# Performance work log

Hardware: AMD Instinct MI355X
Metric: run time of the kernel (lower is better)

The kernel has to match this reference:

```python
import jax, jax.numpy as jnp
import numpy as np


def _lstm_scan(x_tbd, h0, c0, Wi, Wh, b):
    # x_tbd: [T, B, D]; standard LSTMCell, gate order i, f, g, o.
    def step(carry, xt):
        h, c = carry
        gates = xt @ Wi.T + h @ Wh.T + b  # [B, 4H]
        i, f, g, o = jnp.split(gates, 4, axis=-1)
        c = jax.nn.sigmoid(f) * c + jax.nn.sigmoid(i) * jnp.tanh(g)
        h = jax.nn.sigmoid(o) * jnp.tanh(c)
        return (h, c), h
    _, ys = jax.lax.scan(step, (h0, c0), x_tbd)
    return ys  # [T, B, H]


def setup_inputs() -> dict:
    key = jax.random.key(0)
    ks = jax.random.split(key, 8)
    B, T, D, H = 64, 512, 512, 512
    inputs_emb = jax.random.normal(ks[0], (B, T, D), dtype=jnp.float32)
    # variable sequence lengths in [T//2, T], mask = 1 for valid positions
    lengths = jax.random.randint(ks[1], (B,), T // 2, T + 1)
    mask = (jnp.arange(T)[None, :] < lengths[:, None]).astype(jnp.float32)
    s = 1.0 / np.sqrt(H)
    return {
        "inputs_emb": inputs_emb,
        "mask": mask,
        "h0": jnp.zeros((B, H), jnp.float32),
        "c0": jnp.zeros((B, H), jnp.float32),
        "Wi_f": jax.random.uniform(ks[2], (4 * H, D), jnp.float32, -s, s),
        "Wh_f": jax.random.uniform(ks[3], (4 * H, H), jnp.float32, -s, s),
        "b_f": jnp.zeros((4 * H,), jnp.float32),
        "Wi_b": jax.random.uniform(ks[4], (4 * H, D), jnp.float32, -s, s),
        "Wh_b": jax.random.uniform(ks[5], (4 * H, H), jnp.float32, -s, s),
        "b_b": jnp.zeros((4 * H,), jnp.float32),
    }


def reference(inputs_emb, mask, h0, c0, Wi_f, Wh_f, b_f, Wi_b, Wh_b, b_b):
    B, T, D = inputs_emb.shape
    # ---- forward direction ----
    ys_f = _lstm_scan(inputs_emb.transpose(1, 0, 2), h0, c0, Wi_f, Wh_f, b_f)  # [T,B,H]
    out_f = ys_f.transpose(1, 0, 2)  # [B,T,H]
    # ---- backward direction with gather-based reordering ----
    lengths = mask.astype(jnp.int32).sum(axis=1)  # [B]
    t_idx = jnp.arange(T)[None, :]
    # index_b: rotate so padding comes first: [len..T-1] ++ [0..len-1]
    idx_b = (t_idx + lengths[:, None]) % T  # [B,T]
    # index_f: rotate back: [T-len..T-1] ++ [0..T-len-1]
    idx_f = (t_idx + (T - lengths)[:, None]) % T  # [B,T]
    x_b = jnp.take_along_axis(inputs_emb, idx_b[:, :, None], axis=1)  # [B,T,D]
    # run cell over reversed time, then reverse collected outputs back
    x_b_rev = x_b.transpose(1, 0, 2)[::-1]  # [T,B,D], t = T-1 .. 0
    ys_b_rev = _lstm_scan(x_b_rev, h0, c0, Wi_b, Wh_b, b_b)  # [T,B,H]
    out_b = ys_b_rev[::-1].transpose(1, 0, 2)  # [B,T,H], time order
    out_b = jnp.take_along_axis(out_b, idx_f[:, :, None], axis=1)
    return jnp.concatenate([out_f, out_b], axis=-1)  # [B,T,2H]
```

## Files before the change

### kernel.cpp

```cpp
#include <hip/hip_runtime.h>
#include <hip/hip_fp16.h>

typedef _Float16 f16x8 __attribute__((ext_vector_type(8)));
typedef float f32x4 __attribute__((ext_vector_type(4)));

#define TT 512
#define HH 512
#define BB 64

#define WS_LENS  4096
#define WS_HBUF  8192
#define WS_END   (8192 + 524288)

#define LDS_W     0
#define LDS_GLDS  131072
#define LDS_H     135424
#define LDS_TOTAL 151808

#define MFMA(a, b, c) __builtin_amdgcn_mfma_f32_16x16x32_f16((a), (b), (c), 0, 0, 0)

__device__ __forceinline__ float fsig(float x) {
  float ax = __builtin_fabsf(x);
  float t  = __builtin_amdgcn_exp2f(-1.442695041f * ax);
  float r  = __builtin_amdgcn_rcpf(1.0f + t);
  return x >= 0.0f ? r : t * r;
}
__device__ __forceinline__ float ftanh_(float x) {
  float ax = __builtin_fabsf(x);
  float t  = __builtin_amdgcn_exp2f(-2.885390082f * ax);
  float r  = (1.0f - t) * __builtin_amdgcn_rcpf(1.0f + t);
  return x >= 0.0f ? r : -r;
}

__global__ void len_kernel(const float* __restrict__ mask, int* __restrict__ lens) {
  int b = threadIdx.x;
  if (b < BB) {
    float s = 0.f;
    for (int t = 0; t < TT; ++t) s += mask[b * TT + t];
    lens[b] = (int)(s + 0.5f);
  }
}

__global__ void __launch_bounds__(256, 1)
bilstm_kernel(const float* __restrict__ x, const int* __restrict__ lens,
              const float* __restrict__ h0, const float* __restrict__ c0,
              const float* __restrict__ Wi_f, const float* __restrict__ Wh_f,
              const float* __restrict__ b_f,
              const float* __restrict__ Wi_b, const float* __restrict__ Wh_b,
              const float* __restrict__ b_b,
              float* __restrict__ out, unsigned long long* hbuf)
{
  extern __shared__ __align__(16) char smem[];
  f16x8* wlds = (f16x8*)(smem + LDS_W);
  float (*glds)[68] = (float (*)[68])(smem + LDS_GLDS);
  char* htile = smem + LDS_H;

  const int bid = blockIdx.x;
  const int dir = bid >> 7;
  const int bg  = (bid >> 5) & 3;
  const int cg  = bid & 31;
  const int tid = threadIdx.x;
  const int wv  = tid >> 6;
  const int ln  = tid & 63;
  const int il  = ln & 15;
  const int kg  = ln >> 4;

  const float* Wi = dir ? Wi_b : Wi_f;
  const float* Wh = dir ? Wh_b : Wh_f;
  const float* bv = dir ? b_b  : b_f;

  unsigned long long* hb64 = hbuf + (size_t)dir * (2 * BB * 256);

  const int jrow = wv * HH + cg * 16 + il;
#pragma unroll 4
  for (int kk = 0; kk < 32; ++kk) {
    int k0 = kk * 32 + kg * 8;
    const float* src = (k0 < 512) ? (Wi + (size_t)jrow * 512 + k0)
                                  : (Wh + (size_t)jrow * 512 + (k0 - 512));
    float4 f0 = *(const float4*)(src);
    float4 f1 = *(const float4*)(src + 4);
    f16x8 w;
    w[0] = (_Float16)f0.x; w[1] = (_Float16)f0.y; w[2] = (_Float16)f0.z; w[3] = (_Float16)f0.w;
    w[4] = (_Float16)f1.x; w[5] = (_Float16)f1.y; w[6] = (_Float16)f1.z; w[7] = (_Float16)f1.w;
    wlds[(wv * 32 + kk) * 64 + ln] = w;
  }
  const f16x8* wbase = wlds + (size_t)wv * 32 * 64 + ln;

  const int bl_e  = tid >> 4;
  const int i_e   = tid & 15;
  const int b_e   = bg * 16 + bl_e;
  const int col_e = cg * 16 + i_e;
  float cst = c0[(size_t)b_e * HH + col_e];
  const float bi_ = bv[0 * HH + col_e];
  const float bf_ = bv[1 * HH + col_e];
  const float bg_ = bv[2 * HH + col_e];
  const float bo_ = bv[3 * HH + col_e];
  const int len_e = lens[b_e];

  const int b_g   = bg * 16 + il;
  const int len_b = lens[b_g];

  {
    unsigned int hbits = __half_as_ushort(__float2half(h0[(size_t)b_e * HH + col_e]));
    unsigned int pb = __shfl_xor((int)hbits, 1);
    if ((tid & 1) == 0) {
      unsigned long long pw = (1ull << 32) | ((unsigned long long)pb << 16) | hbits;
      __hip_atomic_store(hb64 + (size_t)1 * BB * 256 + (size_t)b_e * 256 + (col_e >> 1), pw,
                         __ATOMIC_RELAXED, __HIP_MEMORY_SCOPE_AGENT);
    }
  }
  __syncthreads();

  for (int t = 0; t < TT; ++t) {
    const unsigned long long* hs = hb64 + (size_t)((t + 1) & 1) * BB * 256 + (size_t)bg * 16 * 256;
    const unsigned int expT = (unsigned int)(t + 1);
    unsigned long long hwv[16];
#pragma unroll
    for (int s = 0; s < 16; ++s)
      hwv[s] = __hip_atomic_load(hs + s * 256 + tid, __ATOMIC_RELAXED, __HIP_MEMORY_SCOPE_AGENT);

    int tsrc;
    if (dir == 0) tsrc = t;
    else { int v = len_b + (TT - 1) - t; if (v >= TT) v -= TT; tsrc = v; }
    const float* xrow = x + ((size_t)b_g * TT + tsrc) * 512;
    f16x8 ax[16];
#pragma unroll
    for (int kk = 0; kk < 16; ++kk) {
      float4 f0 = *(const float4*)(xrow + kk * 32 + kg * 8);
      float4 f1 = *(const float4*)(xrow + kk * 32 + kg * 8 + 4);
      f16x8 w;
      w[0] = (_Float16)f0.x; w[1] = (_Float16)f0.y; w[2] = (_Float16)f0.z; w[3] = (_Float16)f0.w;
      w[4] = (_Float16)f1.x; w[5] = (_Float16)f1.y; w[6] = (_Float16)f1.z; w[7] = (_Float16)f1.w;
      ax[kk] = w;
    }

    f32x4 ac0 = {0.f,0.f,0.f,0.f}, ac1 = {0.f,0.f,0.f,0.f};
    f32x4 ac2 = {0.f,0.f,0.f,0.f}, ac3 = {0.f,0.f,0.f,0.f};
#pragma unroll
    for (int kk = 0; kk < 16; kk += 4) {
      ac0 = MFMA(ax[kk + 0], wbase[(kk + 0) * 64], ac0);
      ac1 = MFMA(ax[kk + 1], wbase[(kk + 1) * 64], ac1);
      ac2 = MFMA(ax[kk + 2], wbase[(kk + 2) * 64], ac2);
      ac3 = MFMA(ax[kk + 3], wbase[(kk + 3) * 64], ac3);
    }

    {
      bool ok = true;
#pragma unroll
      for (int s = 0; s < 16; ++s) ok &= ((unsigned int)(hwv[s] >> 32) == expT);
      while (!__all(ok)) {
        __builtin_amdgcn_s_sleep(2);
#pragma unroll
        for (int s = 0; s < 16; ++s)
          hwv[s] = __hip_atomic_load(hs + s * 256 + tid, __ATOMIC_RELAXED, __HIP_MEMORY_SCOPE_AGENT);
        ok = true;
#pragma unroll
        for (int s = 0; s < 16; ++s) ok &= ((unsigned int)(hwv[s] >> 32) == expT);
      }
    }

#pragma unroll
    for (int s = 0; s < 16; ++s) {
      unsigned int lo = (unsigned int)hwv[s];
      *(unsigned int*)(htile + s * 1024 + ((tid * 4) ^ ((s & 7) << 4))) = lo;
    }
    __syncthreads();

    f16x8 fh[16];
#pragma unroll
    for (int kk = 0; kk < 16; ++kk) {
      int inr = kk * 64 + kg * 16;
      fh[kk] = *(const f16x8*)(htile + il * 1024 + (inr ^ ((il & 7) << 4)));
    }

#pragma unroll
    for (int kk = 0; kk < 16; kk += 4) {
      ac0 = MFMA(fh[kk + 0], wbase[(16 + kk + 0) * 64], ac0);
      ac1 = MFMA(fh[kk + 1], wbase[(16 + kk + 1) * 64], ac1);
      ac2 = MFMA(fh[kk + 2], wbase[(16 + kk + 2) * 64], ac2);
      ac3 = MFMA(fh[kk + 3], wbase[(16 + kk + 3) * 64], ac3);
    }

#pragma unroll
    for (int r = 0; r < 4; ++r)
      glds[kg * 4 + r][wv * 16 + il] = ac0[r] + ac1[r] + ac2[r] + ac3[r];
    __syncthreads();

    float gi = glds[bl_e][ 0 + i_e] + bi_;
    float gf = glds[bl_e][16 + i_e] + bf_;
    float gg = glds[bl_e][32 + i_e] + bg_;
    float go = glds[bl_e][48 + i_e] + bo_;
    float si = fsig(gi), sf = fsig(gf), so = fsig(go);
    float tg = ftanh_(gg);
    cst = sf * cst + si * tg;
    float hv = so * ftanh_(cst);

    {
      unsigned int hbits = __half_as_ushort(__float2half(hv));
      unsigned int pb = __shfl_xor((int)hbits, 1);
      if ((tid & 1) == 0) {
        unsigned long long pw = ((unsigned long long)(unsigned int)(t + 2) << 32)
                              | ((unsigned long long)pb << 16) | hbits;
        __hip_atomic_store(hb64 + (size_t)(t & 1) * BB * 256 + (size_t)b_e * 256 + (col_e >> 1), pw,
                           __ATOMIC_RELAXED, __HIP_MEMORY_SCOPE_AGENT);
      }
    }

    if (dir == 0) {
      out[((size_t)b_e * TT + t) * (2 * HH) + col_e] = hv;
    } else {
      int td = len_e - 1 - t; if (td < 0) td += TT;
      out[((size_t)b_e * TT + td) * (2 * HH) + HH + col_e] = hv;
    }
  }
}

extern "C" void kernel_launch(void* const* d_in, const int* in_sizes, int n_in,
                              void* d_out, int out_size, void* d_ws, size_t ws_size,
                              hipStream_t stream) {
  const float* x    = (const float*)d_in[0];
  const float* mask = (const float*)d_in[1];
  const float* h0   = (const float*)d_in[2];
  const float* c0   = (const float*)d_in[3];
  const float* Wi_f = (const float*)d_in[4];
  const float* Wh_f = (const float*)d_in[5];
  const float* b_f  = (const float*)d_in[6];
  const float* Wi_b = (const float*)d_in[7];
  const float* Wh_b = (const float*)d_in[8];
  const float* b_b  = (const float*)d_in[9];
  float* out = (float*)d_out;

  char* ws = (char*)d_ws;
  int*                lens = (int*)(ws + WS_LENS);
  unsigned long long* hbuf = (unsigned long long*)(ws + WS_HBUF);

  hipMemsetAsync(ws, 0, WS_END, stream);

  hipLaunchKernelGGL(len_kernel, dim3(1), dim3(64), 0, stream, mask, lens);

  hipFuncSetAttribute((const void*)bilstm_kernel,
                      hipFuncAttributeMaxDynamicSharedMemorySize, LDS_TOTAL);

  hipLaunchKernelGGL(bilstm_kernel, dim3(256), dim3(256), LDS_TOTAL, stream,
                     x, lens, h0, c0, Wi_f, Wh_f, b_f, Wi_b, Wh_b, b_b,
                     out, hbuf);
}
```

Before: 3.326 ms.

## Precompute input projections with a batched GEMM and keep weights in registers

Adds a pre-pass that converts x to fp16 and computes the input-to-gate projection for all timesteps and both directions as one large MFMA GEMM into workspace. The recurrent kernel then only adds a precomputed value per gate instead of running the x@Wi MFMAs inside the serial loop. Recurrent weights move from LDS into VGPRs, and the spin-wait sleep is shortened and given a timeout. The gx path needs about 300 MB of workspace and only runs when enough is provided. It also rounds gx to fp16 and adds extra kernel launches and global traffic.

```diff
diff --git a/kernel.cpp b/kernel.cpp
--- a/kernel.cpp
+++ b/kernel.cpp
@@ -10,14 +10,16 @@
 
 #define WS_LENS  4096
 #define WS_HBUF  8192
-#define WS_END   (8192 + 524288)
-
-#define LDS_W     0
-#define LDS_GLDS  131072
-#define LDS_H     135424
-#define LDS_TOTAL 151808
-
-#define MFMA(a, b, c) __builtin_amdgcn_mfma_f32_16x16x32_f16((a), (b), (c), 0, 0, 0)
+#define WS_ZERO  532480
+#define WS_XH    (1u << 20)
+#define WS_GX    36700160u
+#define WS_NEED  305135616ull
+
+#define LDS_HT    0
+#define LDS_GLDS  16384
+#define LDS_TOTAL 90112
+
+#define MFMA(a,b,c) __builtin_amdgcn_mfma_f32_16x16x32_f16((a),(b),(c),0,0,0)
 
 __device__ __forceinline__ float fsig(float x) {
   float ax = __builtin_fabsf(x);
@@ -30,6 +32,13 @@
   float t  = __builtin_amdgcn_exp2f(-2.885390082f * ax);
   float r  = (1.0f - t) * __builtin_amdgcn_rcpf(1.0f + t);
   return x >= 0.0f ? r : -r;
+}
+__device__ __forceinline__ f16x8 cvt8(const float* p) {
+  float4 a = *(const float4*)p, b = *(const float4*)(p + 4);
+  f16x8 w;
+  w[0]=(_Float16)a.x; w[1]=(_Float16)a.y; w[2]=(_Float16)a.z; w[3]=(_Float16)a.w;
+  w[4]=(_Float16)b.x; w[5]=(_Float16)b.y; w[6]=(_Float16)b.z; w[7]=(_Float16)b.w;
+  return w;
 }
 
 __global__ void len_kernel(const float* __restrict__ mask, int* __restrict__ lens) {
@@ -39,6 +48,70 @@
     for (int t = 0; t < TT; ++t) s += mask[b * TT + t];
     lens[b] = (int)(s + 0.5f);
   }
+}
+
+__global__ void cvt_x_kernel(const float* __restrict__ x, __half* __restrict__ xh, int n4) {
+  int i = blockIdx.x * blockDim.x + threadIdx.x;
+  int stride = gridDim.x * blockDim.x;
+  for (; i < n4; i += stride) {
+    float4 v = ((const float4*)x)[i];
+    ushort4 o;
+    o.x = __half_as_ushort(__float2half(v.x));
+    o.y = __half_as_ushort(__float2half(v.y));
+    o.z = __half_as_ushort(__float2half(v.z));
+    o.w = __half_as_ushort(__float2half(v.w));
+    ((ushort4*)xh)[i] = o;
+  }
+}
+
+__global__ void gx_kernel(const __half* __restrict__ xh, const float* __restrict__ Wi_f,
+                          const float* __restrict__ Wi_b, __half* __restrict__ gx) {
+  const int rt = blockIdx.x, ct = blockIdx.y, dir = blockIdx.z;
+  const int tid = threadIdx.x, wv = tid >> 6, ln = tid & 63, il = ln & 15, kg = ln >> 4;
+  const float* wsrc = dir ? Wi_b : Wi_f;
+
+  const int arow = rt * 128 + wv * 32 + il;
+  const __half* ap0 = xh + (size_t)arow * 512 + kg * 8;
+  const __half* ap1 = ap0 + 16 * 512;
+  const float* bp0 = wsrc + (size_t)(ct * 64 +  0 + il) * 512 + kg * 8;
+  const float* bp1 = wsrc + (size_t)(ct * 64 + 16 + il) * 512 + kg * 8;
+  const float* bp2 = wsrc + (size_t)(ct * 64 + 32 + il) * 512 + kg * 8;
+  const float* bp3 = wsrc + (size_t)(ct * 64 + 48 + il) * 512 + kg * 8;
+
+  f32x4 acc[2][4];
+#pragma unroll
+  for (int m = 0; m < 2; ++m)
+#pragma unroll
+    for (int n = 0; n < 4; ++n) acc[m][n] = (f32x4){0.f,0.f,0.f,0.f};
+
+#pragma unroll 4
+  for (int ks = 0; ks < 16; ++ks) {
+    f16x8 a0 = *(const f16x8*)(ap0 + ks * 32);
+    f16x8 a1 = *(const f16x8*)(ap1 + ks * 32);
+    f16x8 b0 = cvt8(bp0 + ks * 32);
+    f16x8 b1 = cvt8(bp1 + ks * 32);
+    f16x8 b2 = cvt8(bp2 + ks * 32);
+    f16x8 b3 = cvt8(bp3 + ks * 32);
+    acc[0][0] = MFMA(a0, b0, acc[0][0]);
+    acc[0][1] = MFMA(a0, b1, acc[0][1]);
+    acc[0][2] = MFMA(a0, b2, acc[0][2]);
+    acc[0][3] = MFMA(a0, b3, acc[0][3]);
+    acc[1][0] = MFMA(a1, b0, acc[1][0]);
+    acc[1][1] = MFMA(a1, b1, acc[1][1]);
+    acc[1][2] = MFMA(a1, b2, acc[1][2]);
+    acc[1][3] = MFMA(a1, b3, acc[1][3]);
+  }
+
+#pragma unroll
+  for (int m = 0; m < 2; ++m)
+#pragma unroll
+    for (int n = 0; n < 4; ++n)
+#pragma unroll
+      for (int r = 0; r < 4; ++r) {
+        int row = rt * 128 + wv * 32 + m * 16 + kg * 4 + r;
+        int col = ct * 64 + n * 16 + il;
+        gx[((size_t)dir * 32768 + row) * 2048 + col] = __float2half(acc[m][n][r]);
+      }
 }
 
 __global__ void __launch_bounds__(256, 1)
@@ -48,22 +121,19 @@
               const float* __restrict__ b_f,
               const float* __restrict__ Wi_b, const float* __restrict__ Wh_b,
               const float* __restrict__ b_b,
-              float* __restrict__ out, unsigned long long* hbuf)
+              float* __restrict__ out, unsigned long long* hbuf,
+              const __half* __restrict__ gx, int has_gx)
 {
   extern __shared__ __align__(16) char smem[];
-  f16x8* wlds = (f16x8*)(smem + LDS_W);
+  char* htile = smem + LDS_HT;
   float (*glds)[68] = (float (*)[68])(smem + LDS_GLDS);
-  char* htile = smem + LDS_H;
 
   const int bid = blockIdx.x;
   const int dir = bid >> 7;
   const int bg  = (bid >> 5) & 3;
   const int cg  = bid & 31;
   const int tid = threadIdx.x;
-  const int wv  = tid >> 6;
-  const int ln  = tid & 63;
-  const int il  = ln & 15;
-  const int kg  = ln >> 4;
+  const int wv  = tid >> 6, ln = tid & 63, il = ln & 15, kg = ln >> 4;
 
   const float* Wi = dir ? Wi_b : Wi_f;
   const float* Wh = dir ? Wh_b : Wh_f;
@@ -72,32 +142,23 @@
   unsigned long long* hb64 = hbuf + (size_t)dir * (2 * BB * 256);
 
   const int jrow = wv * HH + cg * 16 + il;
-#pragma unroll 4
+  f16x8 wreg[32];
+#pragma unroll
   for (int kk = 0; kk < 32; ++kk) {
     int k0 = kk * 32 + kg * 8;
     const float* src = (k0 < 512) ? (Wi + (size_t)jrow * 512 + k0)
                                   : (Wh + (size_t)jrow * 512 + (k0 - 512));
-    float4 f0 = *(const float4*)(src);
-    float4 f1 = *(const float4*)(src + 4);
-    f16x8 w;
-    w[0] = (_Float16)f0.x; w[1] = (_Float16)f0.y; w[2] = (_Float16)f0.z; w[3] = (_Float16)f0.w;
-    w[4] = (_Float16)f1.x; w[5] = (_Float16)f1.y; w[6] = (_Float16)f1.z; w[7] = (_Float16)f1.w;
-    wlds[(wv * 32 + kk) * 64 + ln] = w;
-  }
-  const f16x8* wbase = wlds + (size_t)wv * 32 * 64 + ln;
-
-  const int bl_e  = tid >> 4;
-  const int i_e   = tid & 15;
-  const int b_e   = bg * 16 + bl_e;
-  const int col_e = cg * 16 + i_e;
+    wreg[kk] = cvt8(src);
+  }
+
+  const int bl_e = tid >> 4, i_e = tid & 15;
+  const int b_e = bg * 16 + bl_e, col_e = cg * 16 + i_e;
   float cst = c0[(size_t)b_e * HH + col_e];
-  const float bi_ = bv[0 * HH + col_e];
-  const float bf_ = bv[1 * HH + col_e];
-  const float bg_ = bv[2 * HH + col_e];
-  const float bo_ = bv[3 * HH + col_e];
+  const float bi_ = bv[0*HH+col_e], bf_ = bv[1*HH+col_e],
+              bg_ = bv[2*HH+col_e], bo_ = bv[3*HH+col_e];
   const int len_e = lens[b_e];
 
-  const int b_g   = bg * 16 + il;
+  const int b_g = bg * 16 + il;
   const int len_b = lens[b_g];
 
   {
@@ -112,6 +173,22 @@
   __syncthreads();
 
   for (int t = 0; t < TT; ++t) {
+    if (has_gx) {
+      asm volatile("" : "+v"(wreg[16]),"+v"(wreg[17]),"+v"(wreg[18]),"+v"(wreg[19]),
+                        "+v"(wreg[20]),"+v"(wreg[21]),"+v"(wreg[22]),"+v"(wreg[23]),
+                        "+v"(wreg[24]),"+v"(wreg[25]),"+v"(wreg[26]),"+v"(wreg[27]),
+                        "+v"(wreg[28]),"+v"(wreg[29]),"+v"(wreg[30]),"+v"(wreg[31]));
+    } else {
+      asm volatile("" : "+v"(wreg[0]),"+v"(wreg[1]),"+v"(wreg[2]),"+v"(wreg[3]),
+                        "+v"(wreg[4]),"+v"(wreg[5]),"+v"(wreg[6]),"+v"(wreg[7]),
+                        "+v"(wreg[8]),"+v"(wreg[9]),"+v"(wreg[10]),"+v"(wreg[11]),
+                        "+v"(wreg[12]),"+v"(wreg[13]),"+v"(wreg[14]),"+v"(wreg[15]));
+      asm volatile("" : "+v"(wreg[16]),"+v"(wreg[17]),"+v"(wreg[18]),"+v"(wreg[19]),
+                        "+v"(wreg[20]),"+v"(wreg[21]),"+v"(wreg[22]),"+v"(wreg[23]),
+                        "+v"(wreg[24]),"+v"(wreg[25]),"+v"(wreg[26]),"+v"(wreg[27]),
+                        "+v"(wreg[28]),"+v"(wreg[29]),"+v"(wreg[30]),"+v"(wreg[31]));
+    }
+
     const unsigned long long* hs = hb64 + (size_t)((t + 1) & 1) * BB * 256 + (size_t)bg * 16 * 256;
     const unsigned int expT = (unsigned int)(t + 1);
     unsigned long long hwv[16];
@@ -119,43 +196,52 @@
     for (int s = 0; s < 16; ++s)
       hwv[s] = __hip_atomic_load(hs + s * 256 + tid, __ATOMIC_RELAXED, __HIP_MEMORY_SCOPE_AGENT);
 
-    int tsrc;
-    if (dir == 0) tsrc = t;
-    else { int v = len_b + (TT - 1) - t; if (v >= TT) v -= TT; tsrc = v; }
-    const float* xrow = x + ((size_t)b_g * TT + tsrc) * 512;
-    f16x8 ax[16];
-#pragma unroll
-    for (int kk = 0; kk < 16; ++kk) {
-      float4 f0 = *(const float4*)(xrow + kk * 32 + kg * 8);
-      float4 f1 = *(const float4*)(xrow + kk * 32 + kg * 8 + 4);
-      f16x8 w;
-      w[0] = (_Float16)f0.x; w[1] = (_Float16)f0.y; w[2] = (_Float16)f0.z; w[3] = (_Float16)f0.w;
-      w[4] = (_Float16)f1.x; w[5] = (_Float16)f1.y; w[6] = (_Float16)f1.z; w[7] = (_Float16)f1.w;
-      ax[kk] = w;
-    }
-
     f32x4 ac0 = {0.f,0.f,0.f,0.f}, ac1 = {0.f,0.f,0.f,0.f};
     f32x4 ac2 = {0.f,0.f,0.f,0.f}, ac3 = {0.f,0.f,0.f,0.f};
-#pragma unroll
-    for (int kk = 0; kk < 16; kk += 4) {
-      ac0 = MFMA(ax[kk + 0], wbase[(kk + 0) * 64], ac0);
-      ac1 = MFMA(ax[kk + 1], wbase[(kk + 1) * 64], ac1);
-      ac2 = MFMA(ax[kk + 2], wbase[(kk + 2) * 64], ac2);
-      ac3 = MFMA(ax[kk + 3], wbase[(kk + 3) * 64], ac3);
+
+    float gxa0 = 0.f, gxa1 = 0.f, gxa2 = 0.f, gxa3 = 0.f;
+    if (has_gx) {
+      int tse;
+      if (dir == 0) tse = t;
+      else { int v = len_e + (TT - 1) - t; if (v >= TT) v -= TT; tse = v; }
+      const __half* gp = gx + ((size_t)dir * 32768 + (size_t)b_e * TT + tse) * 2048 + col_e;
+      gxa0 = __half2float(gp[0]);
+      gxa1 = __half2float(gp[512]);
+      gxa2 = __half2float(gp[1024]);
+      gxa3 = __half2float(gp[1536]);
+    } else {
+      int tsrc;
+      if (dir == 0) tsrc = t;
+      else { int v = len_b + (TT - 1) - t; if (v >= TT) v -= TT; tsrc = v; }
+      const float* xrow = x + ((size_t)b_g * TT + tsrc) * 512;
+#pragma unroll
+      for (int kq = 0; kq < 4; ++kq) {
+        f16x8 w0 = cvt8(xrow + (kq*4+0)*32 + kg*8);
+        f16x8 w1 = cvt8(xrow + (kq*4+1)*32 + kg*8);
+        f16x8 w2 = cvt8(xrow + (kq*4+2)*32 + kg*8);
+        f16x8 w3 = cvt8(xrow + (kq*4+3)*32 + kg*8);
+        ac0 = MFMA(w0, wreg[kq*4+0], ac0);
+        ac1 = MFMA(w1, wreg[kq*4+1], ac1);
+        ac2 = MFMA(w2, wreg[kq*4+2], ac2);
+        ac3 = MFMA(w3, wreg[kq*4+3], ac3);
+      }
     }
 
     {
       bool ok = true;
 #pragma unroll
       for (int s = 0; s < 16; ++s) ok &= ((unsigned int)(hwv[s] >> 32) == expT);
+      unsigned long long tspin = 0;
       while (!__all(ok)) {
-        __builtin_amdgcn_s_sleep(2);
+        __builtin_amdgcn_s_sleep(1);
 #pragma unroll
         for (int s = 0; s < 16; ++s)
           hwv[s] = __hip_atomic_load(hs + s * 256 + tid, __ATOMIC_RELAXED, __HIP_MEMORY_SCOPE_AGENT);
         ok = true;
 #pragma unroll
         for (int s = 0; s < 16; ++s) ok &= ((unsigned int)(hwv[s] >> 32) == expT);
+        if (tspin == 0) tspin = __builtin_readcyclecounter();
+        else if (__builtin_readcyclecounter() - tspin > (1ull << 31)) break;
       }
     }
 
@@ -166,30 +252,27 @@
     }
     __syncthreads();
 
-    f16x8 fh[16];
-#pragma unroll
-    for (int kk = 0; kk < 16; ++kk) {
-      int inr = kk * 64 + kg * 16;
-      fh[kk] = *(const f16x8*)(htile + il * 1024 + (inr ^ ((il & 7) << 4)));
-    }
-
 #pragma unroll
     for (int kk = 0; kk < 16; kk += 4) {
-      ac0 = MFMA(fh[kk + 0], wbase[(16 + kk + 0) * 64], ac0);
-      ac1 = MFMA(fh[kk + 1], wbase[(16 + kk + 1) * 64], ac1);
-      ac2 = MFMA(fh[kk + 2], wbase[(16 + kk + 2) * 64], ac2);
-      ac3 = MFMA(fh[kk + 3], wbase[(16 + kk + 3) * 64], ac3);
+      f16x8 h0f = *(const f16x8*)(htile + il * 1024 + (((kk+0)*64 + kg*16) ^ ((il & 7) << 4)));
+      f16x8 h1f = *(const f16x8*)(htile + il * 1024 + (((kk+1)*64 + kg*16) ^ ((il & 7) << 4)));
+      f16x8 h2f = *(const f16x8*)(htile + il * 1024 + (((kk+2)*64 + kg*16) ^ ((il & 7) << 4)));
+      f16x8 h3f = *(const f16x8*)(htile + il * 1024 + (((kk+3)*64 + kg*16) ^ ((il & 7) << 4)));
+      ac0 = MFMA(h0f, wreg[16 + kk + 0], ac0);
+      ac1 = MFMA(h1f, wreg[16 + kk + 1], ac1);
+      ac2 = MFMA(h2f, wreg[16 + kk + 2], ac2);
+      ac3 = MFMA(h3f, wreg[16 + kk + 3], ac3);
     }
 
 #pragma unroll
     for (int r = 0; r < 4; ++r)
-      glds[kg * 4 + r][wv * 16 + il] = ac0[r] + ac1[r] + ac2[r] + ac3[r];
+      glds[kg*4+r][wv*16+il] = ac0[r] + ac1[r] + ac2[r] + ac3[r];
     __syncthreads();
 
-    float gi = glds[bl_e][ 0 + i_e] + bi_;
-    float gf = glds[bl_e][16 + i_e] + bf_;
-    float gg = glds[bl_e][32 + i_e] + bg_;
-    float go = glds[bl_e][48 + i_e] + bo_;
+    float gi = glds[bl_e][ 0 + i_e] + gxa0 + bi_;
+    float gf = glds[bl_e][16 + i_e] + gxa1 + bf_;
+    float gg = glds[bl_e][32 + i_e] + gxa2 + bg_;
+    float go = glds[bl_e][48 + i_e] + gxa3 + bo_;
     float si = fsig(gi), sf = fsig(gf), so = fsig(go);
     float tg = ftanh_(gg);
     cst = sf * cst + si * tg;
@@ -233,15 +316,26 @@
   char* ws = (char*)d_ws;
   int*                lens = (int*)(ws + WS_LENS);
   unsigned long long* hbuf = (unsigned long long*)(ws + WS_HBUF);
-
-  hipMemsetAsync(ws, 0, WS_END, stream);
+  __half*             xh   = (__half*)(ws + WS_XH);
+  __half*             gxb  = (__half*)(ws + WS_GX);
+
+  const int has_gx = (ws_size >= WS_NEED) ? 1 : 0;
+
+  hipMemsetAsync(ws, 0, WS_ZERO, stream);
 
   hipLaunchKernelGGL(len_kernel, dim3(1), dim3(64), 0, stream, mask, lens);
+
+  if (has_gx) {
+    hipLaunchKernelGGL(cvt_x_kernel, dim3(2048), dim3(256), 0, stream,
+                       x, xh, (BB * TT * 512) / 4);
+    hipLaunchKernelGGL(gx_kernel, dim3(256, 32, 2), dim3(256), 0, stream,
+                       xh, Wi_f, Wi_b, gxb);
+  }
 
   hipFuncSetAttribute((const void*)bilstm_kernel,
                       hipFuncAttributeMaxDynamicSharedMemorySize, LDS_TOTAL);
 
   hipLaunchKernelGGL(bilstm_kernel, dim3(256), dim3(256), LDS_TOTAL, stream,
                      x, lens, h0, c0, Wi_f, Wh_f, b_f, Wi_b, Wh_b, b_b,
-                     out, hbuf);
-}
+                     out, hbuf, gxb, has_gx);
+}
```

After: 2.782 ms. 1.2x faster.
